# Kernel tuning notes

Hardware: AMD Instinct MI355X
Metric: run time of the kernel (lower is better)

The kernel has to match this reference:

```python
import jax, jax.numpy as jnp
import numpy as np


def setup_inputs() -> dict:
    key = jax.random.key(0)
    k1, k2 = jax.random.split(key)
    N, h, w, c = 512, 64, 64, 32
    X = jax.random.normal(k1, (N, h, w, c), dtype=jnp.float32)       # inducing 'images'
    theta = jax.random.normal(k2, (N, 6), dtype=jnp.float32)         # per-point affine params
    return {"X": X, "theta": theta}


def reference(X, theta):
    # X: (N, h, w, c); theta: (N, 6) -> affine A: (N, 2, 3)
    N, h, w, c = X.shape
    A = theta.reshape(N, 2, 3)

    # Homogeneous target grid (3, h*w) in [-1, 1] coords ('xy' meshgrid as in source).
    Xt, Yt = jnp.meshgrid(jnp.linspace(-1.0, 1.0, w), jnp.linspace(-1.0, 1.0, h))
    Gt = jnp.stack([Xt.ravel(), Yt.ravel(), jnp.ones(h * w, dtype=jnp.float32)])  # (3, HW)

    # Source sampling coordinates per inducing point: (N, 2, HW)
    Gs = jnp.einsum('nij,jk->nik', A, Gt)
    gx = w * (Gs[:, 0, :] + 1.0) / 2.0   # (N, HW)
    gy = h * (Gs[:, 1, :] + 1.0) / 2.0

    X0 = jnp.clip(jnp.floor(gx).astype(jnp.int32), 0, w - 1)
    X1 = jnp.clip(jnp.floor(gx).astype(jnp.int32) + 1, 0, w - 1)
    Y0 = jnp.clip(jnp.floor(gy).astype(jnp.int32), 0, h - 1)
    Y1 = jnp.clip(jnp.floor(gy).astype(jnp.int32) + 1, 0, h - 1)

    # Bilinear weights computed from clipped corner indices (matches source).
    wa = (X1 - gx) * (Y1 - gy)
    wb = (X1 - gx) * (gy - Y0)
    wc = (gx - X0) * (Y1 - gy)
    wd = (gx - X0) * (gy - Y0)

    Sf = X.reshape(N, h * w, c)

    def gather(yi, xi):
        idx = yi * w + xi                                   # (N, HW); clipped so 'wrap' is a no-op
        return jnp.take_along_axis(Sf, idx[..., None], axis=1)  # (N, HW, c)

    T = (wa[..., None] * gather(Y0, X0)
         + wb[..., None] * gather(Y1, X0)
         + wc[..., None] * gather(Y0, X1)
         + wd[..., None] * gather(Y1, X1))
    return T.reshape(N, h, w, c)
```

## Files before the change

kernel.cpp:

```cpp
#include <hip/hip_runtime.h>

#define NIMG 512
#define H 64
#define W 64
#define C 32
#define HW (H * W)

__device__ __forceinline__ int iclamp(int v, int lo, int hi) {
    return v < lo ? lo : (v > hi ? hi : v);
}

__global__ __launch_bounds__(256) void stn_bilinear_kernel(
    const float* __restrict__ X,
    const float* __restrict__ theta,
    float* __restrict__ out)
{
    const int b    = blockIdx.x;
    const int xcd  = b & 7;
    const int sub  = b >> 3;
    const int n    = xcd * 64 + (sub >> 6);
    const int row  = sub & 63;
    const int col  = threadIdx.x >> 2;
    const int quad = threadIdx.x & 3;

    const float* th = theta + n * 6;
    const double a00 = (double)th[0], a01 = (double)th[1], a02 = (double)th[2];
    const double a10 = (double)th[3], a11 = (double)th[4], a12 = (double)th[5];

    const double step = 2.0 / 63.0;
    const double xj = (col == W - 1) ? 1.0 : ((double)col * step - 1.0);
    const double yi = (row == H - 1) ? 1.0 : ((double)row * step - 1.0);

    const double gs0 = (a00 * xj + a01 * yi) + a02;
    const double gs1 = (a10 * xj + a11 * yi) + a12;
    const double gx = (double)W * (gs0 + 1.0) * 0.5;
    const double gy = (double)H * (gs1 + 1.0) * 0.5;

    double fx = floor(gx);
    double fy = floor(gy);
    fx = fmin(fmax(fx, -1.0e6), 1.0e6);
    fy = fmin(fmax(fy, -1.0e6), 1.0e6);
    const int x0i = (int)fx;
    const int y0i = (int)fy;

    const int X0 = iclamp(x0i,     0, W - 1);
    const int X1 = iclamp(x0i + 1, 0, W - 1);
    const int Y0 = iclamp(y0i,     0, H - 1);
    const int Y1 = iclamp(y0i + 1, 0, H - 1);

    const float dwax = (float)((double)X1 - gx);
    const float dwbx = (float)(gx - (double)X0);
    const float dway = (float)((double)Y1 - gy);
    const float dwby = (float)(gy - (double)Y0);

    const float* img = X + (size_t)n * (HW * C);
    const int cb = quad * 8;

    const float4* pa = (const float4*)(img + (Y0 * W + X0) * C + cb);
    const float4* pb = (const float4*)(img + (Y1 * W + X0) * C + cb);
    const float4* pc = (const float4*)(img + (Y0 * W + X1) * C + cb);
    const float4* pd = (const float4*)(img + (Y1 * W + X1) * C + cb);

    float A[8], B[8], Cv[8], D[8];
    *(float4*)&A[0]  = pa[0];  *(float4*)&A[4]  = pa[1];
    *(float4*)&B[0]  = pb[0];  *(float4*)&B[4]  = pb[1];
    *(float4*)&Cv[0] = pc[0];  *(float4*)&Cv[4] = pc[1];
    *(float4*)&D[0]  = pd[0];  *(float4*)&D[4]  = pd[1];

    float r[8];
#pragma unroll
    for (int k = 0; k < 8; ++k) {
        r[k] = dwax * (dway * A[k] + dwby * B[k])
             + dwbx * (dway * Cv[k] + dwby * D[k]);
    }

    const size_t opix = (size_t)(n * HW + row * W + col);
    float* po = out + opix * C + cb;
    *(float4*)(po)     = *(const float4*)&r[0];
    *(float4*)(po + 4) = *(const float4*)&r[4];
}

extern "C" void kernel_launch(void* const* d_in, const int* in_sizes, int n_in,
                              void* d_out, int out_size, void* d_ws, size_t ws_size,
                              hipStream_t stream) {
    const float* X     = (const float*)d_in[0];
    const float* theta = (const float*)d_in[1];
    float* out         = (float*)d_out;

    const int blocks = NIMG * H;
    hipLaunchKernelGGL(stn_bilinear_kernel, dim3(blocks), dim3(256), 0, stream,
                       X, theta, out);
}
```

Baseline: 434.4 us.

## Stage per-image channel slices in LDS as fp16 and gather bilinear taps from shared memory

Each block now loads one image's 8-channel slice with coalesced reads and stores it in LDS as fp16. The four bilinear taps are then gathered from LDS instead of global memory, and the interpolation runs in packed fp16 arithmetic. The aim is to replace scattered, partly redundant global gathers with a single streaming read per image slice. In exchange, 64KB of LDS per block limits occupancy, the load phase is not overlapped with compute, and fp16 storage and arithmetic reduce accuracy.

```diff
diff --git a/kernel.cpp b/kernel.cpp
--- a/kernel.cpp
+++ b/kernel.cpp
@@ -5,79 +5,108 @@
 #define W 64
 #define C 32
 #define HW (H * W)
+#define TPB 512
+
+typedef _Float16 half8 __attribute__((ext_vector_type(8)));
+typedef _Float16 half4v __attribute__((ext_vector_type(4)));
 
 __device__ __forceinline__ int iclamp(int v, int lo, int hi) {
     return v < lo ? lo : (v > hi ? hi : v);
 }
 
-__global__ __launch_bounds__(256) void stn_bilinear_kernel(
+__device__ __forceinline__ half8 splat8(_Float16 x) {
+    half8 v = {x, x, x, x, x, x, x, x};
+    return v;
+}
+
+__global__ __launch_bounds__(TPB) void stn_bilinear_lds_kernel(
     const float* __restrict__ X,
     const float* __restrict__ theta,
     float* __restrict__ out)
 {
-    const int b    = blockIdx.x;
-    const int xcd  = b & 7;
-    const int sub  = b >> 3;
-    const int n    = xcd * 64 + (sub >> 6);
-    const int row  = sub & 63;
-    const int col  = threadIdx.x >> 2;
-    const int quad = threadIdx.x & 3;
+    __shared__ _Float16 s[HW * 8];
+
+    const int b   = blockIdx.x;
+    const int xcd = b & 7;
+    const int sb  = b >> 3;
+    const int oct = sb & 3;
+    const int n   = xcd + ((sb >> 2) << 3);
+    const int tid = threadIdx.x;
 
     const float* th = theta + n * 6;
     const double a00 = (double)th[0], a01 = (double)th[1], a02 = (double)th[2];
     const double a10 = (double)th[3], a11 = (double)th[4], a12 = (double)th[5];
 
-    const double step = 2.0 / 63.0;
-    const double xj = (col == W - 1) ? 1.0 : ((double)col * step - 1.0);
-    const double yi = (row == H - 1) ? 1.0 : ((double)row * step - 1.0);
+    const float* img = X + (size_t)n * (HW * C) + oct * 8;
 
-    const double gs0 = (a00 * xj + a01 * yi) + a02;
-    const double gs1 = (a10 * xj + a11 * yi) + a12;
-    const double gx = (double)W * (gs0 + 1.0) * 0.5;
-    const double gy = (double)H * (gs1 + 1.0) * 0.5;
-
-    double fx = floor(gx);
-    double fy = floor(gy);
-    fx = fmin(fmax(fx, -1.0e6), 1.0e6);
-    fy = fmin(fmax(fy, -1.0e6), 1.0e6);
-    const int x0i = (int)fx;
-    const int y0i = (int)fy;
-
-    const int X0 = iclamp(x0i,     0, W - 1);
-    const int X1 = iclamp(x0i + 1, 0, W - 1);
-    const int Y0 = iclamp(y0i,     0, H - 1);
-    const int Y1 = iclamp(y0i + 1, 0, H - 1);
-
-    const float dwax = (float)((double)X1 - gx);
-    const float dwbx = (float)(gx - (double)X0);
-    const float dway = (float)((double)Y1 - gy);
-    const float dwby = (float)(gy - (double)Y0);
-
-    const float* img = X + (size_t)n * (HW * C);
-    const int cb = quad * 8;
-
-    const float4* pa = (const float4*)(img + (Y0 * W + X0) * C + cb);
-    const float4* pb = (const float4*)(img + (Y1 * W + X0) * C + cb);
-    const float4* pc = (const float4*)(img + (Y0 * W + X1) * C + cb);
-    const float4* pd = (const float4*)(img + (Y1 * W + X1) * C + cb);
-
-    float A[8], B[8], Cv[8], D[8];
-    *(float4*)&A[0]  = pa[0];  *(float4*)&A[4]  = pa[1];
-    *(float4*)&B[0]  = pb[0];  *(float4*)&B[4]  = pb[1];
-    *(float4*)&Cv[0] = pc[0];  *(float4*)&Cv[4] = pc[1];
-    *(float4*)&D[0]  = pd[0];  *(float4*)&D[4]  = pd[1];
-
-    float r[8];
-#pragma unroll
-    for (int k = 0; k < 8; ++k) {
-        r[k] = dwax * (dway * A[k] + dwby * B[k])
-             + dwbx * (dway * Cv[k] + dwby * D[k]);
+    for (int it = tid; it < HW * 2; it += TPB) {
+        const int p  = it >> 1;
+        const int hf = it & 1;
+        const float4 v = *(const float4*)(img + (size_t)p * C + hf * 4);
+        half4v hv = {( _Float16)v.x, (_Float16)v.y, (_Float16)v.z, (_Float16)v.w};
+        *(half4v*)&s[p * 8 + hf * 4] = hv;
     }
 
-    const size_t opix = (size_t)(n * HW + row * W + col);
-    float* po = out + opix * C + cb;
-    *(float4*)(po)     = *(const float4*)&r[0];
-    *(float4*)(po + 4) = *(const float4*)&r[4];
+    __syncthreads();
+
+    const double step = 2.0 / 63.0;
+
+    float* outb = out + (size_t)n * (HW * C) + oct * 8;
+
+    for (int it = tid; it < HW; it += TPB) {
+        const int row = it >> 6;
+        const int col = it & 63;
+
+        const double xj = (col == W - 1) ? 1.0 : ((double)col * step - 1.0);
+        const double yi = (row == H - 1) ? 1.0 : ((double)row * step - 1.0);
+
+        const double gs0 = (a00 * xj + a01 * yi) + a02;
+        const double gs1 = (a10 * xj + a11 * yi) + a12;
+        const double gx = (double)W * (gs0 + 1.0) * 0.5;
+        const double gy = (double)H * (gs1 + 1.0) * 0.5;
+
+        double fx = floor(gx);
+        double fy = floor(gy);
+        fx = fmin(fmax(fx, -1.0e6), 1.0e6);
+        fy = fmin(fmax(fy, -1.0e6), 1.0e6);
+        const int x0i = (int)fx;
+        const int y0i = (int)fy;
+
+        const int X0 = iclamp(x0i,     0, W - 1);
+        const int X1 = iclamp(x0i + 1, 0, W - 1);
+        const int Y0 = iclamp(y0i,     0, H - 1);
+        const int Y1 = iclamp(y0i + 1, 0, H - 1);
+
+        float wax = (float)((double)X1 - gx);
+        float wbx = (float)(gx - (double)X0);
+        float way = (float)((double)Y1 - gy);
+        float wby = (float)(gy - (double)Y0);
+
+        if (X0 == X1) { wax = 0.0f; wbx = 0.0f; }
+        if (Y0 == Y1) { way = 0.0f; wby = 0.0f; }
+
+        const half8 A  = *(const half8*)&s[(Y0 * W + X0) * 8];
+        const half8 Bv = *(const half8*)&s[(Y1 * W + X0) * 8];
+        const half8 Cv = *(const half8*)&s[(Y0 * W + X1) * 8];
+        const half8 Dv = *(const half8*)&s[(Y1 * W + X1) * 8];
+
+        const half8 vway = splat8((_Float16)way);
+        const half8 vwby = splat8((_Float16)wby);
+        const half8 vwax = splat8((_Float16)wax);
+        const half8 vwbx = splat8((_Float16)wbx);
+
+        const half8 left  = A  * vway + Bv * vwby;
+        const half8 right = Cv * vway + Dv * vwby;
+        const half8 res   = left * vwax + right * vwbx;
+
+        float rf[8];
+#pragma unroll
+        for (int k = 0; k < 8; ++k) rf[k] = (float)res[k];
+
+        float* po = outb + (size_t)it * C;
+        *(float4*)(po)     = make_float4(rf[0], rf[1], rf[2], rf[3]);
+        *(float4*)(po + 4) = make_float4(rf[4], rf[5], rf[6], rf[7]);
+    }
 }
 
 extern "C" void kernel_launch(void* const* d_in, const int* in_sizes, int n_in,
@@ -87,7 +116,7 @@
     const float* theta = (const float*)d_in[1];
     float* out         = (float*)d_out;
 
-    const int blocks = NIMG * H;
-    hipLaunchKernelGGL(stn_bilinear_kernel, dim3(blocks), dim3(256), 0, stream,
+    const int blocks = NIMG * 4;
+    hipLaunchKernelGGL(stn_bilinear_lds_kernel, dim3(blocks), dim3(TPB), 0, stream,
                        X, theta, out);
 }
```

Result: slower. 491.8 us (+13.2%).
